# Kernel optimization log

Measured on AMD Instinct MI355X. Metric: run time of the kernel, lower is better.

## Reference

```python
import jax, jax.numpy as jnp
import numpy as np

N_NODES = 100000
N_EDGES = 600000
N_CLASS = 26
HIDDEN = 128


def setup_inputs() -> dict:
    key = jax.random.key(0)
    ks = jax.random.split(key, 8)
    x = jax.random.normal(ks[0], (N_NODES, N_CLASS), dtype=jnp.float32)
    edge_index = jax.random.randint(ks[1], (2, N_EDGES), 0, N_NODES, dtype=jnp.int64)
    edge_weight = jax.random.uniform(ks[2], (N_EDGES,), dtype=jnp.float32)
    W1 = jax.random.normal(ks[3], (N_CLASS, HIDDEN), dtype=jnp.float32) * (1.0 / np.sqrt(N_CLASS))
    b1 = jnp.zeros((HIDDEN,), dtype=jnp.float32)
    W2 = jax.random.normal(ks[4], (HIDDEN, HIDDEN), dtype=jnp.float32) * (1.0 / np.sqrt(HIDDEN))
    b2 = jnp.zeros((HIDDEN,), dtype=jnp.float32)
    Wfc = jax.random.normal(ks[5], (HIDDEN, N_CLASS), dtype=jnp.float32) * (1.0 / np.sqrt(HIDDEN))
    bfc = jnp.zeros((N_CLASS,), dtype=jnp.float32)
    return {"x": x, "edge_index": edge_index, "edge_weight": edge_weight,
            "W1": W1, "b1": b1, "W2": W2, "b2": b2, "Wfc": Wfc, "bfc": bfc}


def _gcn_norm(edge_index, edge_weight, n_nodes):
    # PyG gcn_norm: add self-loops (weight 1), symmetric deg^-1/2 normalization.
    loop = jnp.arange(n_nodes, dtype=edge_index.dtype)
    row = jnp.concatenate([edge_index[0], loop])  # source
    col = jnp.concatenate([edge_index[1], loop])  # destination
    w = jnp.concatenate([edge_weight, jnp.ones((n_nodes,), edge_weight.dtype)])
    deg = jax.ops.segment_sum(w, col, num_segments=n_nodes)
    d_inv_sqrt = jnp.where(deg > 0, jax.lax.rsqrt(jnp.maximum(deg, 1e-12)), 0.0)
    norm = d_inv_sqrt[row] * w * d_inv_sqrt[col]
    return row, col, norm


def _gcn_conv(x, row, col, norm, W, b, n_nodes):
    h = x @ W                              # [N, out]
    msg = norm[:, None] * h[row]           # gather + scale, [E+N, out]
    out = jax.ops.segment_sum(msg, col, num_segments=n_nodes)  # scatter-add
    return out + b


def reference(x, edge_index, edge_weight, W1, b1, W2, b2, Wfc, bfc):
    n = x.shape[0]
    row, col, norm = _gcn_norm(edge_index, edge_weight, n)
    h = jax.nn.relu(_gcn_conv(x, row, col, norm, W1, b1, n))
    h = jax.nn.relu(_gcn_conv(h, row, col, norm, W2, b2, n))
    return h @ Wfc + bfc
```

## Files before the change

kernel.cpp:

```cpp
#include <hip/hip_runtime.h>

#define NNODES 100000
#define NEDGES 600000
#define NCLASS 26
#define HID    128

#define SHIFT  9
#define BCOLS  512
#define NBKT   196
#define EPB    1024
#define NBE    586
#define NH     (NBKT * NBE)

typedef __attribute__((ext_vector_type(8))) _Float16 f16x8;
typedef __attribute__((ext_vector_type(4))) float f32x4;

__device__ inline unsigned short f2h(float f) {
    union { _Float16 h; unsigned short s; } c;
    c.h = (_Float16)f;
    return c.s;
}
__device__ inline unsigned int packh(float a, float b) {
    return (unsigned int)f2h(a) | ((unsigned int)f2h(b) << 16);
}
__device__ inline float hlo(unsigned int p) {
    union { unsigned short s; _Float16 h; } c;
    c.s = (unsigned short)p;
    return (float)c.h;
}
__device__ inline float hhi(unsigned int p) {
    union { unsigned short s; _Float16 h; } c;
    c.s = (unsigned short)(p >> 16);
    return (float)c.h;
}

__global__ __launch_bounds__(256) void histA_k(const int* __restrict__ col,
                                               int* __restrict__ H) {
    __shared__ int h[NBKT];
    int t = threadIdx.x;
    for (int i = t; i < NBKT; i += 256) h[i] = 0;
    __syncthreads();
    int base = blockIdx.x * EPB;
#pragma unroll
    for (int u = 0; u < 4; u++) {
        int e = base + t + u * 256;
        if (e < NEDGES) atomicAdd(&h[col[e] >> SHIFT], 1);
    }
    __syncthreads();
    for (int i = t; i < NBKT; i += 256) H[i * NBE + blockIdx.x] = h[i];
}

__global__ void scanH1_k(const int* __restrict__ in, int* __restrict__ incl,
                         int* __restrict__ aux, int n) {
    __shared__ int s[256];
    int t = threadIdx.x, gi = blockIdx.x * 256 + t;
    s[t] = (gi < n) ? in[gi] : 0;
    __syncthreads();
    for (int off = 1; off < 256; off <<= 1) {
        int x = (t >= off) ? s[t - off] : 0;
        __syncthreads();
        s[t] += x;
        __syncthreads();
    }
    if (gi < n) incl[gi] = s[t];
    if (t == 255) aux[blockIdx.x] = s[255];
}

__global__ void scan2_k(int* __restrict__ aux, int n) {
    __shared__ int s[512];
    int t = threadIdx.x;
    s[t] = (t < n) ? aux[t] : 0;
    __syncthreads();
    for (int off = 1; off < 512; off <<= 1) {
        int x = (t >= off) ? s[t - off] : 0;
        __syncthreads();
        s[t] += x;
        __syncthreads();
    }
    if (t < n) aux[t] = s[t];
}

__device__ inline int exoff(const int* __restrict__ incl, const int* __restrict__ H,
                            const int* __restrict__ aux, int gi) {
    int add = (gi >= 256) ? aux[(gi >> 8) - 1] : 0;
    return incl[gi] - H[gi] + add;
}

__global__ __launch_bounds__(256) void partB_k(const int* __restrict__ row,
                                               const int* __restrict__ col,
                                               const float* __restrict__ w,
                                               const int* __restrict__ incl,
                                               const int* __restrict__ H,
                                               const int* __restrict__ aux,
                                               uint2* __restrict__ rw,
                                               unsigned short* __restrict__ lc) {
    __shared__ int off[NBKT];
    __shared__ int cur[NBKT];
    int t = threadIdx.x;
    for (int i = t; i < NBKT; i += 256) {
        off[i] = exoff(incl, H, aux, i * NBE + blockIdx.x);
        cur[i] = 0;
    }
    __syncthreads();
    int base = blockIdx.x * EPB;
#pragma unroll
    for (int u = 0; u < 4; u++) {
        int e = base + t + u * 256;
        if (e < NEDGES) {
            int c = col[e], b = c >> SHIFT;
            int p = off[b] + atomicAdd(&cur[b], 1);
            rw[p] = make_uint2((unsigned int)row[e], __float_as_uint(w[e]));
            lc[p] = (unsigned short)(c & (BCOLS - 1));
        }
    }
}

__global__ __launch_bounds__(256) void segbp_k(const uint2* __restrict__ rw,
                                               const unsigned short* __restrict__ lc,
                                               const int* __restrict__ incl,
                                               const int* __restrict__ H,
                                               const int* __restrict__ aux,
                                               int* __restrict__ rowptr,
                                               float* __restrict__ dis,
                                               uint2* __restrict__ meta) {
    __shared__ int   cnt[BCOLS];
    __shared__ float ws[BCOLS];
    __shared__ int   rpl[BCOLS];
    __shared__ int   ps[256];
    int b = blockIdx.x, t = threadIdx.x;
    int c0 = b << SHIFT;
    int ncols = min(BCOLS, NNODES - c0);
    for (int i = t; i < BCOLS; i += 256) { cnt[i] = 0; ws[i] = 0.f; }
    __syncthreads();
    int s    = exoff(incl, H, aux, b * NBE);
    int eend = (b == NBKT - 1) ? NEDGES : exoff(incl, H, aux, (b + 1) * NBE);
    for (int e = s + t; e < eend; e += 256) {
        uint2 m = rw[e];
        int l = lc[e];
        atomicAdd(&cnt[l], 1);
        atomicAdd(&ws[l], __uint_as_float(m.y));
    }
    __syncthreads();
    for (int i = t; i < ncols; i += 256) dis[c0 + i] = rsqrtf(1.0f + ws[i]);
    int a0 = cnt[2 * t], a1 = cnt[2 * t + 1];
    ps[t] = a0 + a1;
    __syncthreads();
    for (int off = 1; off < 256; off <<= 1) {
        int x = (t >= off) ? ps[t - off] : 0;
        __syncthreads();
        ps[t] += x;
        __syncthreads();
    }
    int ex = (t > 0) ? ps[t - 1] : 0;
    rpl[2 * t]     = s + ex;
    rpl[2 * t + 1] = s + ex + a0;
    if (2 * t     < ncols) rowptr[c0 + 2 * t]     = s + ex;
    if (2 * t + 1 < ncols) rowptr[c0 + 2 * t + 1] = s + ex + a0;
    if (b == NBKT - 1 && t == 0) rowptr[NNODES] = NEDGES;
    cnt[2 * t] = 0; cnt[2 * t + 1] = 0;
    __syncthreads();
    for (int e = s + t; e < eend; e += 256) {
        uint2 m = rw[e];
        int l = lc[e];
        int pos = rpl[l] + atomicAdd(&cnt[l], 1);
        meta[pos] = make_uint2(m.x, m.y);
    }
}

__global__ __launch_bounds__(256) void prep_k(const float* __restrict__ W2,
                                              const float* __restrict__ W1,
                                              const float* __restrict__ Wfc,
                                              const float* __restrict__ x,
                                              const float* __restrict__ dis,
                                              unsigned short* __restrict__ wt,
                                              unsigned short* __restrict__ w1t,
                                              unsigned short* __restrict__ wfct,
                                              unsigned int* __restrict__ xp) {
    int b = blockIdx.x, t = threadIdx.x;
    if (b < 64) {
        int idx = b * 256 + t;
        int c = idx >> 7, k = idx & 127;
        wt[c * 128 + k] = f2h(W2[k * 128 + c]);
    } else if (b < 80) {
        int idx = (b - 64) * 256 + t;
        int c = idx >> 5, k = idx & 31;
        w1t[c * 32 + k] = (k < NCLASS) ? f2h(W1[k * 128 + c]) : (unsigned short)0;
    } else if (b < 96) {
        int idx = (b - 80) * 256 + t;
        int c = idx >> 7, k = idx & 127;
        wfct[c * 128 + k] = (c < NCLASS) ? f2h(Wfc[k * NCLASS + c]) : (unsigned short)0;
    } else {
        int i = (b - 96) * 256 + t;
        if (i < NNODES * 16) {
            int r = i >> 4, u = i & 15, f0 = u * 2;
            float d = dis[r];
            float a = (f0     < NCLASS) ? x[r * NCLASS + f0]     : 0.f;
            float c = (f0 + 1 < NCLASS) ? x[r * NCLASS + f0 + 1] : 0.f;
            xp[i] = packh(d * a, d * c);
        }
    }
}

__global__ __launch_bounds__(256) void agg26_k(const int* __restrict__ rowptr,
                                               const uint2* __restrict__ meta,
                                               const unsigned int* __restrict__ xp,
                                               const float* __restrict__ dis,
                                               unsigned int* __restrict__ aggx) {
    int node = blockIdx.x * 16 + (threadIdx.x >> 4);
    int lane = threadIdx.x & 15;

    unsigned int self = xp[node * 16 + lane];
    float2 acc = make_float2(hlo(self), hhi(self));
    int j = rowptr[node], jend = rowptr[node + 1];
    for (; j + 3 < jend; j += 4) {
        uint2 m0 = meta[j],     m1 = meta[j + 1];
        uint2 m2 = meta[j + 2], m3 = meta[j + 3];
        unsigned int g0 = xp[m0.x * 16 + lane];
        unsigned int g1 = xp[m1.x * 16 + lane];
        unsigned int g2 = xp[m2.x * 16 + lane];
        unsigned int g3 = xp[m3.x * 16 + lane];
        float v0 = __uint_as_float(m0.y), v1 = __uint_as_float(m1.y);
        float v2 = __uint_as_float(m2.y), v3 = __uint_as_float(m3.y);
        acc.x = fmaf(v0, hlo(g0), acc.x); acc.y = fmaf(v0, hhi(g0), acc.y);
        acc.x = fmaf(v1, hlo(g1), acc.x); acc.y = fmaf(v1, hhi(g1), acc.y);
        acc.x = fmaf(v2, hlo(g2), acc.x); acc.y = fmaf(v2, hhi(g2), acc.y);
        acc.x = fmaf(v3, hlo(g3), acc.x); acc.y = fmaf(v3, hhi(g3), acc.y);
    }
    for (; j < jend; j++) {
        uint2 m = meta[j];
        float v = __uint_as_float(m.y);
        unsigned int g = xp[m.x * 16 + lane];
        acc.x = fmaf(v, hlo(g), acc.x); acc.y = fmaf(v, hhi(g), acc.y);
    }
    float d = dis[node];
    aggx[node * 16 + lane] = packh(d * acc.x, d * acc.y);
}

__global__ __launch_bounds__(256) void gemm12_k(const unsigned short* __restrict__ aggx,
                                                const unsigned short* __restrict__ w1t,
                                                const float* __restrict__ b1,
                                                const unsigned short* __restrict__ wt,
                                                const float* __restrict__ dis,
                                                unsigned short* __restrict__ C, int N) {
    __shared__ unsigned short h1s[64 * 136];
    __shared__ unsigned short Ws[128 * 72];
    const int tid  = threadIdx.x;
    const int wv = tid >> 6, lane = tid & 63;
    const int quad = lane >> 4, l16 = lane & 15;
    const int row0 = blockIdx.x * 64;
    const int wrow = wv * 16;

#pragma unroll
    for (int jj = 0; jj < 4; jj++) {
        int idx = tid + jj * 256;
        int r = idx >> 3, ku = idx & 7;
        *(uint4*)&Ws[r * 72 + ku * 8] = *(const uint4*)&wt[(size_t)r * 128 + ku * 8];
    }

    {
        int ar = row0 + wrow + l16;
        f16x8 af1 = (ar < N) ? *(const f16x8*)&aggx[(size_t)ar * 32 + quad * 8]
                             : (f16x8)(_Float16)0.f;
#pragma unroll
        for (int n = 0; n < 8; n++) {
            f16x8 bw = *(const f16x8*)&w1t[(n * 16 + l16) * 32 + quad * 8];
            f32x4 hacc = __builtin_amdgcn_mfma_f32_16x16x32_f16(af1, bw, (f32x4)0.f, 0, 0, 0);
            int col = n * 16 + l16;
            float bv = b1[col];
#pragma unroll
            for (int r = 0; r < 4; r++)
                h1s[(wrow + quad * 4 + r) * 136 + col] = f2h(fmaxf(hacc[r] + bv, 0.f));
        }
    }
    __syncthreads();

    f16x8 af[4];
#pragma unroll
    for (int kc = 0; kc < 4; kc++)
        af[kc] = *(const f16x8*)&h1s[(wrow + l16) * 136 + kc * 32 + quad * 8];

    f32x4 acc[8];
#pragma unroll
    for (int n = 0; n < 8; n++) acc[n] = (f32x4)0.f;

    for (int c = 0; c < 2; c++) {
        if (c == 1) {
            __syncthreads();
#pragma unroll
            for (int jj = 0; jj < 4; jj++) {
                int idx = tid + jj * 256;
                int r = idx >> 3, ku = idx & 7;
                *(uint4*)&Ws[r * 72 + ku * 8] =
                    *(const uint4*)&wt[(size_t)r * 128 + 64 + ku * 8];
            }
            __syncthreads();
        }
#pragma unroll
        for (int n = 0; n < 8; n++) {
#pragma unroll
            for (int kc = 0; kc < 2; kc++) {
                f16x8 bfr = *(const f16x8*)&Ws[(n * 16 + l16) * 72 + kc * 32 + quad * 8];
                acc[n] = __builtin_amdgcn_mfma_f32_16x16x32_f16(
                    af[c * 2 + kc], bfr, acc[n], 0, 0, 0);
            }
        }
    }

    const int rbase = row0 + wrow + quad * 4;
    float dv[4];
#pragma unroll
    for (int r = 0; r < 4; r++)
        dv[r] = (rbase + r < N) ? dis[rbase + r] : 0.f;
#pragma unroll
    for (int n = 0; n < 8; n++) {
        int col = n * 16 + l16;
#pragma unroll
        for (int r = 0; r < 4; r++) {
            if (rbase + r < N)
                C[(size_t)(rbase + r) * 128 + col] = f2h(dv[r] * acc[n][r]);
        }
    }
}

__global__ __launch_bounds__(256) void aggfc_k(const int* __restrict__ rowptr,
                                               const uint2* __restrict__ meta,
                                               const uint2* __restrict__ h,
                                               const float* __restrict__ dis,
                                               const float* __restrict__ b2,
                                               const unsigned short* __restrict__ wfct,
                                               const float* __restrict__ bfc,
                                               float* __restrict__ out, int N) {
    __shared__ unsigned short h2s[64 * 136];
    const int tid = threadIdx.x;
    const int wv = tid >> 6, lane = tid & 63;
    const int l32 = lane & 31, sub = lane >> 5;
    const int nbase = blockIdx.x * 64;

#pragma unroll 2
    for (int p = 0; p < 8; p++) {
        int r = wv * 16 + p * 2 + sub;
        int node = nbase + r;
        float4 acc = make_float4(0.f, 0.f, 0.f, 0.f);
        float d = 0.f;
        if (node < N) {
            d = dis[node];
            uint2 hcu = h[(size_t)node * 32 + l32];
            acc.x = hlo(hcu.x); acc.y = hhi(hcu.x);
            acc.z = hlo(hcu.y); acc.w = hhi(hcu.y);
            int j = rowptr[node], jend = rowptr[node + 1];
            for (; j + 3 < jend; j += 4) {
                uint2 m0 = meta[j],     m1 = meta[j + 1];
                uint2 m2 = meta[j + 2], m3 = meta[j + 3];
                uint2 g0 = h[(size_t)m0.x * 32 + l32];
                uint2 g1 = h[(size_t)m1.x * 32 + l32];
                uint2 g2 = h[(size_t)m2.x * 32 + l32];
                uint2 g3 = h[(size_t)m3.x * 32 + l32];
                float v0 = __uint_as_float(m0.y), v1 = __uint_as_float(m1.y);
                float v2 = __uint_as_float(m2.y), v3 = __uint_as_float(m3.y);
                acc.x = fmaf(v0, hlo(g0.x), acc.x); acc.y = fmaf(v0, hhi(g0.x), acc.y);
                acc.z = fmaf(v0, hlo(g0.y), acc.z); acc.w = fmaf(v0, hhi(g0.y), acc.w);
                acc.x = fmaf(v1, hlo(g1.x), acc.x); acc.y = fmaf(v1, hhi(g1.x), acc.y);
                acc.z = fmaf(v1, hlo(g1.y), acc.z); acc.w = fmaf(v1, hhi(g1.y), acc.w);
                acc.x = fmaf(v2, hlo(g2.x), acc.x); acc.y = fmaf(v2, hhi(g2.x), acc.y);
                acc.z = fmaf(v2, hlo(g2.y), acc.z); acc.w = fmaf(v2, hhi(g2.y), acc.w);
                acc.x = fmaf(v3, hlo(g3.x), acc.x); acc.y = fmaf(v3, hhi(g3.x), acc.y);
                acc.z = fmaf(v3, hlo(g3.y), acc.z); acc.w = fmaf(v3, hhi(g3.y), acc.w);
            }
            for (; j < jend; j++) {
                uint2 m = meta[j];
                float v = __uint_as_float(m.y);
                uint2 g = h[(size_t)m.x * 32 + l32];
                acc.x = fmaf(v, hlo(g.x), acc.x); acc.y = fmaf(v, hhi(g.x), acc.y);
                acc.z = fmaf(v, hlo(g.y), acc.z); acc.w = fmaf(v, hhi(g.y), acc.w);
            }
        }
        float4 bv = ((const float4*)b2)[l32];
        acc.x = fmaxf(fmaf(d, acc.x, bv.x), 0.f);
        acc.y = fmaxf(fmaf(d, acc.y, bv.y), 0.f);
        acc.z = fmaxf(fmaf(d, acc.z, bv.z), 0.f);
        acc.w = fmaxf(fmaf(d, acc.w, bv.w), 0.f);
        if (node >= N) { acc = make_float4(0.f, 0.f, 0.f, 0.f); }
        *(uint2*)&h2s[r * 136 + l32 * 4] =
            make_uint2(packh(acc.x, acc.y), packh(acc.z, acc.w));
    }

    const int q = lane >> 4, m = lane & 15;
    f16x8 af[4];
#pragma unroll
    for (int ks = 0; ks < 4; ks++)
        af[ks] = *(const f16x8*)&h2s[(wv * 16 + m) * 136 + ks * 32 + q * 8];

#pragma unroll
    for (int n = 0; n < 2; n++) {
        f32x4 o = (f32x4)0.f;
#pragma unroll
        for (int ks = 0; ks < 4; ks++) {
            f16x8 bfr = *(const f16x8*)&wfct[(size_t)(n * 16 + m) * 128 + ks * 32 + q * 8];
            o = __builtin_amdgcn_mfma_f32_16x16x32_f16(af[ks], bfr, o, 0, 0, 0);
        }
        int col = n * 16 + m;
        if (col < NCLASS) {
            float bv = bfc[col];
            int r0 = nbase + wv * 16 + q * 4;
#pragma unroll
            for (int r = 0; r < 4; r++) {
                if (r0 + r < N)
                    out[(size_t)(r0 + r) * NCLASS + col] = o[r] + bv;
            }
        }
    }
}

extern "C" void kernel_launch(void* const* d_in, const int* in_sizes, int n_in,
                              void* d_out, int out_size, void* d_ws, size_t ws_size,
                              hipStream_t stream) {
    const float* x   = (const float*)d_in[0];
    const int*   ei  = (const int*)d_in[1];
    const float* ew  = (const float*)d_in[2];
    const float* W1  = (const float*)d_in[3];
    const float* b1  = (const float*)d_in[4];
    const float* W2  = (const float*)d_in[5];
    const float* b2  = (const float*)d_in[6];
    const float* Wfc = (const float*)d_in[7];
    const float* bfc = (const float*)d_in[8];
    float* out = (float*)d_out;

    const int N = NNODES;
    const int* erow = ei;
    const int* ecol = ei + NEDGES;

    float* fws    = (float*)d_ws;
    float* dis    = fws;
    int*   rowptr = (int*)(fws + 100000);
    int*   H      = (int*)(fws + 200004);
    int*   incl   = (int*)(fws + 314860);
    int*   aux    = (int*)(fws + 429716);
    uint2* rw     = (uint2*)(fws + 430228);
    unsigned short* lc = (unsigned short*)(fws + 1630228);
    uint2* meta   = (uint2*)(fws + 1930228);
    unsigned short* wt16   = (unsigned short*)(fws + 3130228);
    unsigned short* w1t16  = (unsigned short*)(fws + 3138420);
    unsigned short* wfct16 = (unsigned short*)(fws + 3140468);
    unsigned int*   xp     = (unsigned int*)(fws + 3142516);
    unsigned int*   aggx   = (unsigned int*)(fws + 4742516);
    unsigned short* hB16   = (unsigned short*)(fws + 6342516);

    const int gScan = (NH + 255) / 256;
    const int gA26  = N / 16;
    const int gPrep = 96 + (N * 16 + 255) / 256;
    const int g64   = (N + 63) / 64;

    histA_k<<<NBE, 256, 0, stream>>>(ecol, H);
    scanH1_k<<<gScan, 256, 0, stream>>>(H, incl, aux, NH);
    scan2_k<<<1, 512, 0, stream>>>(aux, gScan);
    partB_k<<<NBE, 256, 0, stream>>>(erow, ecol, ew, incl, H, aux, rw, lc);
    segbp_k<<<NBKT, 256, 0, stream>>>(rw, lc, incl, H, aux, rowptr, dis, meta);

    prep_k<<<gPrep, 256, 0, stream>>>(W2, W1, Wfc, x, dis, wt16, w1t16, wfct16, xp);

    agg26_k<<<gA26, 256, 0, stream>>>(rowptr, meta, xp, dis, aggx);
    gemm12_k<<<g64, 256, 0, stream>>>((const unsigned short*)aggx, w1t16, b1,
                                      wt16, dis, hB16, N);

    aggfc_k<<<g64, 256, 0, stream>>>(rowptr, meta, (const uint2*)hB16, dis, b2,
                                     wfct16, bfc, out, N);
}
```

Before: 202.6 us.

## Widen per-lane feature vectors in both aggregation kernels to cut lanes per node

```diff
diff --git a/kernel.cpp b/kernel.cpp
--- a/kernel.cpp
+++ b/kernel.cpp
@@ -32,6 +32,17 @@
     union { unsigned short s; _Float16 h; } c;
     c.s = (unsigned short)(p >> 16);
     return (float)c.h;
+}
+
+__device__ inline void fma16(float* acc, float v, uint4 g0, uint4 g1) {
+    acc[0]  = fmaf(v, hlo(g0.x), acc[0]);  acc[1]  = fmaf(v, hhi(g0.x), acc[1]);
+    acc[2]  = fmaf(v, hlo(g0.y), acc[2]);  acc[3]  = fmaf(v, hhi(g0.y), acc[3]);
+    acc[4]  = fmaf(v, hlo(g0.z), acc[4]);  acc[5]  = fmaf(v, hhi(g0.z), acc[5]);
+    acc[6]  = fmaf(v, hlo(g0.w), acc[6]);  acc[7]  = fmaf(v, hhi(g0.w), acc[7]);
+    acc[8]  = fmaf(v, hlo(g1.x), acc[8]);  acc[9]  = fmaf(v, hhi(g1.x), acc[9]);
+    acc[10] = fmaf(v, hlo(g1.y), acc[10]); acc[11] = fmaf(v, hhi(g1.y), acc[11]);
+    acc[12] = fmaf(v, hlo(g1.z), acc[12]); acc[13] = fmaf(v, hhi(g1.z), acc[13]);
+    acc[14] = fmaf(v, hlo(g1.w), acc[14]); acc[15] = fmaf(v, hhi(g1.w), acc[15]);
 }
 
 __global__ __launch_bounds__(256) void histA_k(const int* __restrict__ col,
@@ -206,34 +217,23 @@
                                                const unsigned int* __restrict__ xp,
                                                const float* __restrict__ dis,
                                                unsigned int* __restrict__ aggx) {
-    int node = blockIdx.x * 16 + (threadIdx.x >> 4);
-    int lane = threadIdx.x & 15;
-
-    unsigned int self = xp[node * 16 + lane];
-    float2 acc = make_float2(hlo(self), hhi(self));
+    int node = blockIdx.x * 32 + (threadIdx.x >> 3);
+    int l8 = threadIdx.x & 7;
+    const uint2* xp2 = (const uint2*)xp;
+
+    uint2 self = xp2[(size_t)node * 8 + l8];
+    float acc[4] = { hlo(self.x), hhi(self.x), hlo(self.y), hhi(self.y) };
     int j = rowptr[node], jend = rowptr[node + 1];
-    for (; j + 3 < jend; j += 4) {
-        uint2 m0 = meta[j],     m1 = meta[j + 1];
-        uint2 m2 = meta[j + 2], m3 = meta[j + 3];
-        unsigned int g0 = xp[m0.x * 16 + lane];
-        unsigned int g1 = xp[m1.x * 16 + lane];
-        unsigned int g2 = xp[m2.x * 16 + lane];
-        unsigned int g3 = xp[m3.x * 16 + lane];
-        float v0 = __uint_as_float(m0.y), v1 = __uint_as_float(m1.y);
-        float v2 = __uint_as_float(m2.y), v3 = __uint_as_float(m3.y);
-        acc.x = fmaf(v0, hlo(g0), acc.x); acc.y = fmaf(v0, hhi(g0), acc.y);
-        acc.x = fmaf(v1, hlo(g1), acc.x); acc.y = fmaf(v1, hhi(g1), acc.y);
-        acc.x = fmaf(v2, hlo(g2), acc.x); acc.y = fmaf(v2, hhi(g2), acc.y);
-        acc.x = fmaf(v3, hlo(g3), acc.x); acc.y = fmaf(v3, hhi(g3), acc.y);
-    }
     for (; j < jend; j++) {
         uint2 m = meta[j];
+        uint2 g = xp2[(size_t)m.x * 8 + l8];
         float v = __uint_as_float(m.y);
-        unsigned int g = xp[m.x * 16 + lane];
-        acc.x = fmaf(v, hlo(g), acc.x); acc.y = fmaf(v, hhi(g), acc.y);
+        acc[0] = fmaf(v, hlo(g.x), acc[0]); acc[1] = fmaf(v, hhi(g.x), acc[1]);
+        acc[2] = fmaf(v, hlo(g.y), acc[2]); acc[3] = fmaf(v, hhi(g.y), acc[3]);
     }
     float d = dis[node];
-    aggx[node * 16 + lane] = packh(d * acc.x, d * acc.y);
+    ((uint2*)aggx)[(size_t)node * 8 + l8] =
+        make_uint2(packh(d * acc[0], d * acc[1]), packh(d * acc[2], d * acc[3]));
 }
 
 __global__ __launch_bounds__(256) void gemm12_k(const unsigned short* __restrict__ aggx,
@@ -324,7 +324,7 @@
 
 __global__ __launch_bounds__(256) void aggfc_k(const int* __restrict__ rowptr,
                                                const uint2* __restrict__ meta,
-                                               const uint2* __restrict__ h,
+                                               const uint4* __restrict__ h4,
                                                const float* __restrict__ dis,
                                                const float* __restrict__ b2,
                                                const unsigned short* __restrict__ wfct,
@@ -333,55 +333,53 @@
     __shared__ unsigned short h2s[64 * 136];
     const int tid = threadIdx.x;
     const int wv = tid >> 6, lane = tid & 63;
-    const int l32 = lane & 31, sub = lane >> 5;
+    const int grp = lane >> 3, l8 = lane & 7;
     const int nbase = blockIdx.x * 64;
 
-#pragma unroll 2
-    for (int p = 0; p < 8; p++) {
-        int r = wv * 16 + p * 2 + sub;
+    for (int p = 0; p < 2; p++) {
+        int r = wv * 16 + p * 8 + grp;
         int node = nbase + r;
-        float4 acc = make_float4(0.f, 0.f, 0.f, 0.f);
+        float acc[16];
         float d = 0.f;
         if (node < N) {
             d = dis[node];
-            uint2 hcu = h[(size_t)node * 32 + l32];
-            acc.x = hlo(hcu.x); acc.y = hhi(hcu.x);
-            acc.z = hlo(hcu.y); acc.w = hhi(hcu.y);
+            uint4 s0 = h4[(size_t)node * 16 + l8 * 2];
+            uint4 s1 = h4[(size_t)node * 16 + l8 * 2 + 1];
+            acc[0]  = hlo(s0.x); acc[1]  = hhi(s0.x);
+            acc[2]  = hlo(s0.y); acc[3]  = hhi(s0.y);
+            acc[4]  = hlo(s0.z); acc[5]  = hhi(s0.z);
+            acc[6]  = hlo(s0.w); acc[7]  = hhi(s0.w);
+            acc[8]  = hlo(s1.x); acc[9]  = hhi(s1.x);
+            acc[10] = hlo(s1.y); acc[11] = hhi(s1.y);
+            acc[12] = hlo(s1.z); acc[13] = hhi(s1.z);
+            acc[14] = hlo(s1.w); acc[15] = hhi(s1.w);
             int j = rowptr[node], jend = rowptr[node + 1];
-            for (; j + 3 < jend; j += 4) {
-                uint2 m0 = meta[j],     m1 = meta[j + 1];
-                uint2 m2 = meta[j + 2], m3 = meta[j + 3];
-                uint2 g0 = h[(size_t)m0.x * 32 + l32];
-                uint2 g1 = h[(size_t)m1.x * 32 + l32];
-                uint2 g2 = h[(size_t)m2.x * 32 + l32];
-                uint2 g3 = h[(size_t)m3.x * 32 + l32];
-                float v0 = __uint_as_float(m0.y), v1 = __uint_as_float(m1.y);
-                float v2 = __uint_as_float(m2.y), v3 = __uint_as_float(m3.y);
-                acc.x = fmaf(v0, hlo(g0.x), acc.x); acc.y = fmaf(v0, hhi(g0.x), acc.y);
-                acc.z = fmaf(v0, hlo(g0.y), acc.z); acc.w = fmaf(v0, hhi(g0.y), acc.w);
-                acc.x = fmaf(v1, hlo(g1.x), acc.x); acc.y = fmaf(v1, hhi(g1.x), acc.y);
-                acc.z = fmaf(v1, hlo(g1.y), acc.z); acc.w = fmaf(v1, hhi(g1.y), acc.w);
-                acc.x = fmaf(v2, hlo(g2.x), acc.x); acc.y = fmaf(v2, hhi(g2.x), acc.y);
-                acc.z = fmaf(v2, hlo(g2.y), acc.z); acc.w = fmaf(v2, hhi(g2.y), acc.w);
-                acc.x = fmaf(v3, hlo(g3.x), acc.x); acc.y = fmaf(v3, hhi(g3.x), acc.y);
-                acc.z = fmaf(v3, hlo(g3.y), acc.z); acc.w = fmaf(v3, hhi(g3.y), acc.w);
-            }
             for (; j < jend; j++) {
                 uint2 m = meta[j];
-                float v = __uint_as_float(m.y);
-                uint2 g = h[(size_t)m.x * 32 + l32];
-                acc.x = fmaf(v, hlo(g.x), acc.x); acc.y = fmaf(v, hhi(g.x), acc.y);
-                acc.z = fmaf(v, hlo(g.y), acc.z); acc.w = fmaf(v, hhi(g.y), acc.w);
+                uint4 g0 = h4[(size_t)m.x * 16 + l8 * 2];
+                uint4 g1 = h4[(size_t)m.x * 16 + l8 * 2 + 1];
+                fma16(acc, __uint_as_float(m.y), g0, g1);
             }
-        }
-        float4 bv = ((const float4*)b2)[l32];
-        acc.x = fmaxf(fmaf(d, acc.x, bv.x), 0.f);
-        acc.y = fmaxf(fmaf(d, acc.y, bv.y), 0.f);
-        acc.z = fmaxf(fmaf(d, acc.z, bv.z), 0.f);
-        acc.w = fmaxf(fmaf(d, acc.w, bv.w), 0.f);
-        if (node >= N) { acc = make_float4(0.f, 0.f, 0.f, 0.f); }
-        *(uint2*)&h2s[r * 136 + l32 * 4] =
-            make_uint2(packh(acc.x, acc.y), packh(acc.z, acc.w));
+        } else {
+#pragma unroll
+            for (int k = 0; k < 16; k++) acc[k] = 0.f;
+        }
+        unsigned int wpk[8];
+#pragma unroll
+        for (int q = 0; q < 4; q++) {
+            float4 bv = ((const float4*)b2)[l8 * 4 + q];
+            float a0 = fmaxf(fmaf(d, acc[q * 4 + 0], bv.x), 0.f);
+            float a1 = fmaxf(fmaf(d, acc[q * 4 + 1], bv.y), 0.f);
+            float a2 = fmaxf(fmaf(d, acc[q * 4 + 2], bv.z), 0.f);
+            float a3 = fmaxf(fmaf(d, acc[q * 4 + 3], bv.w), 0.f);
+            if (node >= N) { a0 = a1 = a2 = a3 = 0.f; }
+            wpk[q * 2]     = packh(a0, a1);
+            wpk[q * 2 + 1] = packh(a2, a3);
+        }
+        *(uint4*)&h2s[r * 136 + l8 * 16] =
+            make_uint4(wpk[0], wpk[1], wpk[2], wpk[3]);
+        *(uint4*)&h2s[r * 136 + l8 * 16 + 8] =
+            make_uint4(wpk[4], wpk[5], wpk[6], wpk[7]);
     }
 
     const int q = lane >> 4, m = lane & 15;
@@ -446,7 +444,7 @@
     unsigned short* hB16   = (unsigned short*)(fws + 6342516);
 
     const int gScan = (NH + 255) / 256;
-    const int gA26  = N / 16;
+    const int gA26  = N / 32;
     const int gPrep = 96 + (N * 16 + 255) / 256;
     const int g64   = (N + 63) / 64;
 
@@ -462,6 +460,6 @@
     gemm12_k<<<g64, 256, 0, stream>>>((const unsigned short*)aggx, w1t16, b1,
                                       wt16, dis, hB16, N);
 
-    aggfc_k<<<g64, 256, 0, stream>>>(rowptr, meta, (const uint2*)hB16, dis, b2,
+    aggfc_k<<<g64, 256, 0, stream>>>(rowptr, meta, (const uint4*)hB16, dis, b2,
                                      wfct16, bfc, out, N);
 }
```

After: 201.0 us. About the same (-0.8%).
